# Kernel tuning notes

Measured on AMD Instinct MI355X. Metric: run time of the kernel, lower is better.

The kernel has to match this reference:

```python
import jax, jax.numpy as jnp
import numpy as np
from jax import lax

HIDDEN_DIM = 256


def _conv(x, w, b, stride):
    # x: [B,T,H,W,Cin], w: [1,kh,kw,Cin,Cout]
    y = lax.conv_general_dilated(
        x, w, window_strides=(1, stride, stride), padding='SAME',
        dimension_numbers=('NDHWC', 'DHWIO', 'NDHWC'))
    return y + b


def _encode(video, w1, b1, w2, b2, w3, b3):
    x = video / 255.0
    x = jax.nn.relu(_conv(x, w1, b1, 2))
    x = jax.nn.relu(_conv(x, w2, b2, 2))
    x = jax.nn.relu(_conv(x, w3, b3, 2))
    return x  # [B,T,H/8,W/8,HIDDEN_DIM]


def _sample_features(features, t_idx, y_idx, x_idx):
    # Bilinear sample features[b, t_idx, y_idx, x_idx] -> [B,N,C]
    B, T, H, W, C = features.shape
    t = jnp.clip(t_idx, 0, T - 1)
    y0 = jnp.clip(jnp.floor(y_idx).astype(jnp.int32), 0, H - 1)
    y1 = jnp.clip(y0 + 1, 0, H - 1)
    x0 = jnp.clip(jnp.floor(x_idx).astype(jnp.int32), 0, W - 1)
    x1 = jnp.clip(x0 + 1, 0, W - 1)
    wy1 = y_idx - y0.astype(features.dtype)
    wy0 = 1.0 - wy1
    wx1 = x_idx - x0.astype(features.dtype)
    wx0 = 1.0 - wx1
    bi = jnp.arange(B)[:, None]
    f00 = features[bi, t, y0, x0]
    f01 = features[bi, t, y0, x1]
    f10 = features[bi, t, y1, x0]
    f11 = features[bi, t, y1, x1]
    f0 = f00 * wx0[..., None] + f01 * wx1[..., None]
    f1 = f10 * wx0[..., None] + f11 * wx1[..., None]
    return f0 * wy0[..., None] + f1 * wy1[..., None]


def _forward(video, query_points, w1, b1, w2, b2, w3, b3):
    B, T, H, W, _ = video.shape
    N = query_points.shape[1]
    x = _encode(video, w1, b1, w2, b2, w3, b3)
    feat_H, feat_W = x.shape[2], x.shape[3]
    query_t = (query_points[:, :, 0] * (T - 1)).astype(jnp.int32)
    query_y = query_points[:, :, 1] * (feat_H - 1)
    query_x = query_points[:, :, 2] * (feat_W - 1)
    q = _sample_features(x, query_t, query_y, query_x)  # [B,N,C]
    # dense correlation volume [B,N,T,fH,fW]
    corr = jnp.einsum('bnc,bthwc->bnthw', q, x) / jnp.sqrt(jnp.float32(HIDDEN_DIM))
    probs = jax.nn.softmax(corr.reshape(B, N, T, feat_H * feat_W) * 10.0, axis=-1)
    yy, xx = jnp.meshgrid(jnp.arange(feat_H, dtype=x.dtype),
                          jnp.arange(feat_W, dtype=x.dtype), indexing='ij')
    coords_flat = jnp.stack([xx.flatten(), yy.flatten()], axis=-1)  # [fH*fW, 2]
    pred = jnp.einsum('bntk,kc->bntc', probs, coords_flat)
    pred = pred.at[..., 0].set(pred[..., 0] * (W / feat_W))
    pred = pred.at[..., 1].set(pred[..., 1] * (H / feat_H))
    occlusion = jax.nn.sigmoid(-jnp.max(corr, axis=(-2, -1)))  # [B,N,T]
    return pred, occlusion


def setup_inputs() -> dict:
    key = jax.random.key(0)
    ks = jax.random.split(key, 10)
    B, T, H, W, N = 2, 24, 256, 256, 512
    video = jax.random.uniform(ks[0], (B, T, H, W, 3), jnp.float32) * 255.0
    query_points = jax.random.uniform(ks[1], (B, N, 3), jnp.float32)
    s = 0.05
    w1 = jax.random.normal(ks[2], (1, 7, 7, 3, 64), jnp.float32) * s
    b1 = jnp.zeros((64,), jnp.float32)
    w2 = jax.random.normal(ks[3], (1, 3, 3, 64, 128), jnp.float32) * s
    b2 = jnp.zeros((128,), jnp.float32)
    w3 = jax.random.normal(ks[4], (1, 3, 3, 128, HIDDEN_DIM), jnp.float32) * s
    b3 = jnp.zeros((HIDDEN_DIM,), jnp.float32)
    return {'video': video, 'query_points': query_points,
            'w1': w1, 'b1': b1, 'w2': w2, 'b2': b2, 'w3': w3, 'b3': b3}


def reference(video, query_points, w1, b1, w2, b2, w3, b3):
    return _forward(video, query_points, w1, b1, w2, b2, w3, b3)
```

## Files before the change

### kernel.cpp

```cpp
#include <hip/hip_runtime.h>
#include <hip/hip_bf16.h>
#include <cstdint>
#include <cstddef>


typedef __attribute__((ext_vector_type(8))) short bf16x8;
typedef __attribute__((ext_vector_type(4))) float f32x4;

typedef const __attribute__((address_space(1))) void gv_t;
typedef __attribute__((address_space(3))) void sv_t;

__device__ __forceinline__ unsigned short bfr(float f) {
    return (unsigned short)(__bfloat16_as_ushort(__float2bfloat16(f)));
}

__global__ __launch_bounds__(256) void k_prep(const float* __restrict__ video,
                                              const float* __restrict__ w1,
                                              const float* __restrict__ w2,
                                              const float* __restrict__ w3,
                                              __hip_bfloat16* __restrict__ pv,
                                              unsigned short* __restrict__ c2p,
                                              __hip_bfloat16* __restrict__ wp1,
                                              __hip_bfloat16* __restrict__ wp2,
                                              __hip_bfloat16* __restrict__ wp3)
{
    const int bid = blockIdx.x;
    if (bid < 12288) {
        const int xcd = bid & 7;
        const int sub = bid >> 3;
        const int bt  = xcd * 6 + (sub >> 8);
        const int iy  = sub & 255;
        const int ix = threadIdx.x;
        const float* src = video + ((size_t)(bt * 256 + iy) * 256 + ix) * 3;
        unsigned* dst = (unsigned*)(pv + ((size_t)(bt * 261) + iy + 2) * 1056);
        const float v0 = src[0], v1 = src[1], v2 = src[2];
        const unsigned lo = (unsigned)bfr(v0) | ((unsigned)bfr(v1) << 16);
        const unsigned hi = (unsigned)bfr(v2);
        dst[(2 + ix) * 2 + 0] = lo;
        dst[(2 + ix) * 2 + 1] = hi;
        if (ix < 2)   { dst[ix * 2] = 0u; dst[ix * 2 + 1] = 0u; }
        if (ix >= 250){ dst[(ix + 8) * 2] = 0u; dst[(ix + 8) * 2 + 1] = 0u; }
    } else if (bid < 12288 + 4086) {
        const int i = (bid - 12288) * 256 + threadIdx.x;
        unsigned short* pvs = (unsigned short*)pv;
        if (i < 253440) {
            const int bt = i / 5280, rr = (i % 5280) / 1056, col = i % 1056;
            const int row = (rr < 2) ? rr : rr + 256;
            pvs[(size_t)(bt * 261 + row) * 1056 + col] = 0;
        } else {
            const int j = i - 253440, bt = j / 16512, k = j % 16512;
            size_t addr;
            if (k < 8320) { const int px = k >> 7, c = k & 127;
                addr = ((size_t)(bt * 65 + 64) * 65 + px) * 128 + c; }
            else { const int k2 = k - 8320, row = k2 >> 7, c = k2 & 127;
                addr = ((size_t)(bt * 65 + row) * 65 + 64) * 128 + c; }
            c2p[addr] = 0;
        }
    } else {
        const int e = (bid - 12288 - 4086) * 256 + threadIdx.x;
        if (e < 14336) {
            const int j = e & 7, lane = (e >> 3) & 63, nt = (e >> 9) & 3, kh = e >> 11;
            const int k = ((lane >> 4) << 3) + j;
            const int kw = k >> 2, ci = k & 3;
            const int n = nt * 16 + (lane & 15);
            float v = (ci < 3 && kw < 7) ? w1[(size_t)((kh * 7 + kw) * 3 + ci) * 64 + n] : 0.f;
            wp1[e] = __float2bfloat16(v);
        } else if (e < 88064) {
            const int e2 = e - 14336;
            const int j = e2 & 7, lane = (e2 >> 3) & 63, nt = (e2 >> 9) & 7, ks = (e2 >> 12) & 1, tap = e2 >> 13;
            const int ci = ks * 32 + ((lane >> 4) << 3) + j;
            const int n  = nt * 16 + (lane & 15);
            wp2[e2] = __float2bfloat16(w2[(size_t)(tap * 64 + ci) * 128 + n]);
        } else {
            const int e3 = e - 88064;
            const int j = e3 & 7, lane = (e3 >> 3) & 63, nt = (e3 >> 9) & 15, ks = (e3 >> 13) & 3, tap = e3 >> 15;
            const int ci = ks * 32 + ((lane >> 4) << 3) + j;
            const int n  = nt * 16 + (lane & 15);
            wp3[e3] = __float2bfloat16(w3[(size_t)(tap * 128 + ci) * 256 + n]);
        }
    }
}

__global__ __launch_bounds__(256, 2) void k_conv12(const __hip_bfloat16* __restrict__ pv,
                                                   const __hip_bfloat16* __restrict__ w1p,
                                                   const float* __restrict__ b1,
                                                   const __hip_bfloat16* __restrict__ w2p,
                                                   const float* __restrict__ b2,
                                                   __hip_bfloat16* __restrict__ c2p)
{
    __shared__ __align__(16) char lc1[3 * 16512];

    const int xcd = blockIdx.x & 7;
    const int sub = blockIdx.x >> 3;
    const int bt  = xcd * 6 + sub / 64;
    const int oy2 = sub % 64;
    const int tid = threadIdx.x;
    const int w   = tid >> 6;
    const int l   = tid & 63;
    const int li  = l & 15, lh = l >> 4;

    const short* pvS = (const short*)pv;
    const short* w1S = (const short*)w1p;

    const int r0 = oy2 * 2;
    f32x4 acc1[3][2][4];
#pragma unroll
    for (int row = 0; row < 3; ++row)
#pragma unroll
        for (int m = 0; m < 2; ++m)
#pragma unroll
            for (int n = 0; n < 4; ++n) acc1[row][m][n] = (f32x4){0.f, 0.f, 0.f, 0.f};

    const int ox0 = w * 32;
#pragma unroll
    for (int kh = 0; kh < 7; ++kh) {
        bf16x8 bw[4];
#pragma unroll
        for (int nt = 0; nt < 4; ++nt)
            bw[nt] = *reinterpret_cast<const bf16x8*>(w1S + ((size_t)(kh * 4 + nt) * 64 + l) * 8);
#pragma unroll
        for (int row = 0; row < 3; ++row) {
            const int r   = r0 + row;
            const int rcl = (r < 128) ? r : 127;
            const short* rbase = pvS + (size_t)(bt * 261 + rcl * 2 + kh) * 1056;
#pragma unroll
            for (int mt = 0; mt < 2; ++mt) {
                bf16x8 a = *reinterpret_cast<const bf16x8*>(
                    rbase + 8 * (ox0 + mt * 16 + li + lh));
#pragma unroll
                for (int nt = 0; nt < 4; ++nt)
                    acc1[row][mt][nt] = __builtin_amdgcn_mfma_f32_16x16x32_bf16(
                        a, bw[nt], acc1[row][mt][nt], 0, 0, 0);
            }
        }
    }

#pragma unroll
    for (int row = 0; row < 3; ++row) {
        const int r = r0 + row;
        char* rowbuf = lc1 + row * 16512;
        if (r < 128) {
#pragma unroll
            for (int mt = 0; mt < 2; ++mt) {
#pragma unroll
                for (int nt = 0; nt < 4; ++nt) {
                    const int n = nt * 16 + li;
                    const float bias = b1[n];
                    const int jg = nt * 2 + (li >> 3);
#pragma unroll
                    for (int r4 = 0; r4 < 4; ++r4) {
                        const int px = ox0 + mt * 16 + lh * 4 + r4;
                        const float v = fmaxf(acc1[row][mt][nt][r4] * (1.f / 255.f) + bias, 0.f);
                        *reinterpret_cast<unsigned short*>(
                            rowbuf + px * 128 + ((jg ^ ((px >> 1) & 7)) * 16 + (li & 7) * 2)) = bfr(v);
                    }
                }
            }
            if (tid < 8)
                *reinterpret_cast<uint4*>(rowbuf + 128 * 128 + tid * 16) = (uint4){0u, 0u, 0u, 0u};
        } else {
#pragma unroll
            for (int it = 0; it < 5; ++it) {
                const int g = it * 256 + tid;
                if (g < 1032)
                    *reinterpret_cast<uint4*>(rowbuf + (size_t)g * 16) = (uint4){0u, 0u, 0u, 0u};
            }
        }
    }
    __syncthreads();

    const int ntb = w * 2;
    f32x4 acc[4][2];
#pragma unroll
    for (int i = 0; i < 4; ++i) {
        acc[i][0] = (f32x4){0.f, 0.f, 0.f, 0.f};
        acc[i][1] = (f32x4){0.f, 0.f, 0.f, 0.f};
    }

    const char* wB = (const char*)w2p;
#pragma unroll
    for (int s = 0; s < 18; ++s) {
        const int tap = s >> 1, ks = s & 1;
        const int kh = tap / 3, kw = tap % 3;

        bf16x8 bf[2];
#pragma unroll
        for (int j = 0; j < 2; ++j)
            bf[j] = *reinterpret_cast<const bf16x8*>(wB + ((size_t)s * 8 + ntb + j) * 1024 + l * 16);

        const char* Ar = lc1 + kh * 16512;
        bf16x8 af[4];
#pragma unroll
        for (int i = 0; i < 4; ++i) {
            const int ix  = (i * 16 + li) * 2 + kw;
            const int off = ((ks * 4 + lh) ^ ((ix >> 1) & 7)) * 16;
            af[i] = *reinterpret_cast<const bf16x8*>(Ar + (size_t)ix * 128 + off);
        }

#pragma unroll
        for (int i = 0; i < 4; ++i)
#pragma unroll
            for (int j = 0; j < 2; ++j)
                acc[i][j] = __builtin_amdgcn_mfma_f32_16x16x32_bf16(af[i], bf[j], acc[i][j], 0, 0, 0);
    }

    __hip_bfloat16* ob = c2p + (size_t)(bt * 65 + oy2) * 65 * 128;
#pragma unroll
    for (int i = 0; i < 4; ++i) {
        const int ox = i * 16 + lh * 4;
#pragma unroll
        for (int j = 0; j < 2; ++j) {
            const int n = (ntb + j) * 16 + li;
            const float bv = b2[n];
#pragma unroll
            for (int r4 = 0; r4 < 4; ++r4) {
                const float v = fmaxf(acc[i][j][r4] + bv, 0.f);
                ob[(size_t)(ox + r4) * 128 + n] = __float2bfloat16(v);
            }
        }
    }
}

template<int CIN, int COUT, int OW, int IW, int ORS, int NTHR, int WMT, int WNT, int MINW>
__global__ __launch_bounds__(NTHR, MINW) void k_convr(const __hip_bfloat16* __restrict__ in,
                                                      const __hip_bfloat16* __restrict__ wp,
                                                      const float* __restrict__ bias,
                                                      __hip_bfloat16* __restrict__ out)
{
    constexpr int KSN  = CIN / 32;
    constexpr int NSL  = 9 * KSN;
    constexpr int NTT  = COUT / 16;
    constexpr int GPX  = CIN / 8;
    constexpr int ROWG = IW * GPX;
    constexpr int RST  = ROWG * 16;
    constexpr int TOT  = 3 * ROWG;
    constexpr int SIT  = (TOT + NTHR - 1) / NTHR;

    __shared__ char lbuf[3 * RST];

    const int bid = blockIdx.x;
    const int xcd = bid & 7;
    const int sub = bid >> 3;
    const int bt  = xcd * 6 + sub / OW;
    const int oy  = sub % OW;

    const int tid = threadIdx.x;
    const int w   = tid >> 6;
    const int l   = tid & 63;
    const int li  = l & 15, lh = l >> 4;
    const int ntb = w * WNT;

    const short* inS = (const short*)in;
    const size_t rb = (size_t)(bt * IW + oy * 2) * IW * CIN;
#pragma unroll
    for (int it = 0; it < SIT; ++it) {
        const int g = it * NTHR + tid;
        if (g < TOT) {
            const int r  = g / ROWG;
            const int rm = g - r * ROWG;
            const int px = rm / GPX;
            const int j  = rm - px * GPX;
            const int q  = j ^ ((px >> 1) & 7);
            __builtin_amdgcn_global_load_lds(
                (gv_t*)(inS + rb + (size_t)r * IW * CIN + px * CIN + q * 8),
                (sv_t*)(lbuf + (size_t)g * 16), 16, 0, 0);
        }
    }
    __syncthreads();

    f32x4 acc[WMT][WNT];
#pragma unroll
    for (int i = 0; i < WMT; ++i)
#pragma unroll
        for (int j = 0; j < WNT; ++j) acc[i][j] = (f32x4){0.f, 0.f, 0.f, 0.f};

    const char* wB = (const char*)wp;

#pragma unroll
    for (int s = 0; s < NSL; ++s) {
        const int tap = s / KSN, ks = s % KSN;
        const int kh = tap / 3, kw = tap % 3;

        bf16x8 bf[WNT];
#pragma unroll
        for (int j = 0; j < WNT; ++j)
            bf[j] = *reinterpret_cast<const bf16x8*>(wB + ((size_t)s * NTT + ntb + j) * 1024 + l * 16);

        const char* Ar = lbuf + kh * RST;
        bf16x8 af[WMT];
#pragma unroll
        for (int i = 0; i < WMT; ++i) {
            const int ix  = (i * 16 + li) * 2 + kw;
            const int off = ((ks * 4 + lh) ^ ((ix >> 1) & 7)) * 16;
            af[i] = *reinterpret_cast<const bf16x8*>(Ar + (size_t)ix * (CIN * 2) + off);
        }

#pragma unroll
        for (int i = 0; i < WMT; ++i)
#pragma unroll
            for (int j = 0; j < WNT; ++j)
                acc[i][j] = __builtin_amdgcn_mfma_f32_16x16x32_bf16(af[i], bf[j], acc[i][j], 0, 0, 0);
    }

    __hip_bfloat16* ob = out + (size_t)(bt * ORS + oy) * ORS * COUT;
#pragma unroll
    for (int i = 0; i < WMT; ++i) {
        const int ox = i * 16 + lh * 4;
#pragma unroll
        for (int j = 0; j < WNT; ++j) {
            const int n = (ntb + j) * 16 + li;
            const float bv = bias[n];
#pragma unroll
            for (int r = 0; r < 4; ++r) {
                const float v = fmaxf(acc[i][j][r] + bv, 0.f);
                ob[(size_t)(ox + r) * COUT + n] = __float2bfloat16(v);
            }
        }
    }
}

__global__ __launch_bounds__(256) void k_sample(const float* __restrict__ qp,
                                                const __hip_bfloat16* __restrict__ feat,
                                                __hip_bfloat16* __restrict__ q)
{
    const int bn = blockIdx.x;
    const int b  = bn >> 9;
    const float t3 = qp[bn * 3 + 0];
    const float yv = qp[bn * 3 + 1] * 31.f;
    const float xv = qp[bn * 3 + 2] * 31.f;
    int t = (int)(t3 * 23.f);
    t = min(max(t, 0), 23);
    int y0 = (int)floorf(yv); y0 = min(max(y0, 0), 31);
    const int y1 = min(y0 + 1, 31);
    int x0 = (int)floorf(xv); x0 = min(max(x0, 0), 31);
    const int x1 = min(x0 + 1, 31);
    const float wy1 = yv - (float)y0, wy0 = 1.f - wy1;
    const float wx1 = xv - (float)x0, wx0 = 1.f - wx1;

    const int c = threadIdx.x;
    const __hip_bfloat16* fb = feat + ((size_t)(b * 24 + t) * 1024) * 256;
    const float f00 = __bfloat162float(fb[(size_t)(y0 * 32 + x0) * 256 + c]);
    const float f01 = __bfloat162float(fb[(size_t)(y0 * 32 + x1) * 256 + c]);
    const float f10 = __bfloat162float(fb[(size_t)(y1 * 32 + x0) * 256 + c]);
    const float f11 = __bfloat162float(fb[(size_t)(y1 * 32 + x1) * 256 + c]);
    const float v = (f00 * wx0 + f01 * wx1) * wy0 + (f10 * wx0 + f11 * wx1) * wy1;
    q[(size_t)bn * 256 + c] = __float2bfloat16(v);
}

__global__ __launch_bounds__(256, 2) void k_corrm(const __hip_bfloat16* __restrict__ qb,
                                                  const __hip_bfloat16* __restrict__ featb,
                                                  float* __restrict__ pbuf)
{
    __shared__ short lbuf[2][8192];

    const int bid = blockIdx.x;
    const int xcd = bid & 7;
    const int sub = bid >> 3;
    const int grp = sub >> 5;
    const int prt = sub & 31;
    const int img = xcd * 6 + grp;
    const int bq  = img / 24, t = img % 24;
    const int nc  = prt & 3, ps = prt >> 2;

    const int tid = threadIdx.x;
    const int w   = tid >> 6;
    const int l   = tid & 63;
    const int li  = l & 15, lh = l >> 4;

    const short* qS = (const short*)qb;
    const short* fS = (const short*)featb + (size_t)img * 1024 * 256;
    const char*  tile0 = (const char*)(fS + (size_t)(ps * 128) * 256);

    const int q0 = nc * 128 + w * 32;
    bf16x8 aq[2][8];
#pragma unroll
    for (int mt = 0; mt < 2; ++mt)
#pragma unroll
        for (int ks = 0; ks < 8; ++ks)
            aq[mt][ks] = *reinterpret_cast<const bf16x8*>(
                qS + ((size_t)(bq * 512 + q0 + mt * 16 + li)) * 256 + ks * 32 + lh * 8);

    float m[2][4], s[2][4], sx[2][4], sy[2][4], dmx[2][4];
#pragma unroll
    for (int mt = 0; mt < 2; ++mt)
#pragma unroll
        for (int r = 0; r < 4; ++r) {
            m[mt][r] = -1e30f; s[mt][r] = 0.f; sx[mt][r] = 0.f; sy[mt][r] = 0.f; dmx[mt][r] = -1e30f;
        }

    bf16x8 stg[4];
#pragma unroll
    for (int i = 0; i < 4; ++i) {
        const int g = i * 256 + tid;
        const int pos = g >> 5, kb = (g & 31) * 16;
        stg[i] = *reinterpret_cast<const bf16x8*>(tile0 + (size_t)pos * 512 + kb);
    }
#pragma unroll
    for (int i = 0; i < 4; ++i) {
        const int g = i * 256 + tid;
        const int pos = g >> 5, kb = (g & 31) * 16;
        *reinterpret_cast<bf16x8*>((char*)&lbuf[0][0] + pos * 512 + (kb ^ ((pos & 7) << 4))) = stg[i];
    }
    __syncthreads();

#pragma unroll
    for (int st = 0; st < 4; ++st) {
        const int cur = st & 1;

        if (st < 3) {
            const char* tn = tile0 + (size_t)((st + 1) * 32) * 512;
#pragma unroll
            for (int i = 0; i < 4; ++i) {
                const int g = i * 256 + tid;
                const int pos = g >> 5, kb = (g & 31) * 16;
                stg[i] = *reinterpret_cast<const bf16x8*>(tn + (size_t)pos * 512 + kb);
            }
        }

        f32x4 acc[2][2];
#pragma unroll
        for (int mt = 0; mt < 2; ++mt)
#pragma unroll
            for (int pt = 0; pt < 2; ++pt) acc[mt][pt] = (f32x4){0.f, 0.f, 0.f, 0.f};

#pragma unroll
        for (int pt = 0; pt < 2; ++pt) {
            const int p = pt * 16 + li;
#pragma unroll
            for (int ks = 0; ks < 8; ++ks) {
                const int k = ks * 32 + lh * 8;
                bf16x8 bv = *reinterpret_cast<const bf16x8*>(&lbuf[cur][p * 256 + (k ^ ((p & 7) << 3))]);
                acc[0][pt] = __builtin_amdgcn_mfma_f32_16x16x32_bf16(aq[0][ks], bv, acc[0][pt], 0, 0, 0);
                acc[1][pt] = __builtin_amdgcn_mfma_f32_16x16x32_bf16(aq[1][ks], bv, acc[1][pt], 0, 0, 0);
            }
        }

        const float py = (float)(ps * 4 + st);
#pragma unroll
        for (int mt = 0; mt < 2; ++mt)
#pragma unroll
            for (int r = 0; r < 4; ++r) {
                const float v0 = acc[mt][0][r], v1 = acc[mt][1][r];
                float mx = fmaxf(v0, v1);
                mx = fmaxf(mx, __shfl_xor(mx, 1));
                mx = fmaxf(mx, __shfl_xor(mx, 2));
                mx = fmaxf(mx, __shfl_xor(mx, 4));
                mx = fmaxf(mx, __shfl_xor(mx, 8));
                dmx[mt][r] = fmaxf(dmx[mt][r], mx);
                const float mn = fmaxf(m[mt][r], mx * 0.625f);
                const float sc = __expf(m[mt][r] - mn);
                const float e0 = __expf(v0 * 0.625f - mn);
                const float e1 = __expf(v1 * 0.625f - mn);
                const float es = e0 + e1;
                s[mt][r]  = s[mt][r]  * sc + es;
                sx[mt][r] = sx[mt][r] * sc + es * (float)li + 16.f * e1;
                sy[mt][r] = sy[mt][r] * sc + es * py;
                m[mt][r] = mn;
            }

        if (st < 3) {
#pragma unroll
            for (int i = 0; i < 4; ++i) {
                const int g = i * 256 + tid;
                const int pos = g >> 5, kb = (g & 31) * 16;
                *reinterpret_cast<bf16x8*>((char*)&lbuf[cur ^ 1][0] + pos * 512 + (kb ^ ((pos & 7) << 4))) = stg[i];
            }
            __syncthreads();
        }
    }

#pragma unroll
    for (int mt = 0; mt < 2; ++mt)
#pragma unroll
        for (int r = 0; r < 4; ++r) {
#pragma unroll
            for (int off = 1; off < 16; off <<= 1) {
                s[mt][r]  += __shfl_xor(s[mt][r],  off);
                sx[mt][r] += __shfl_xor(sx[mt][r], off);
                sy[mt][r] += __shfl_xor(sy[mt][r], off);
            }
        }

    if (li == 0) {
#pragma unroll
        for (int mt = 0; mt < 2; ++mt)
#pragma unroll
            for (int r = 0; r < 4; ++r) {
                const int n = q0 + mt * 16 + lh * 4 + r;
                const int bnt = (bq * 512 + n) * 24 + t;
                const int pi = ps * 24576 + bnt;
                pbuf[pi]                = m[mt][r];
                pbuf[196608 + pi]       = s[mt][r];
                pbuf[393216 + pi]       = sx[mt][r];
                pbuf[589824 + pi]       = sy[mt][r];
                pbuf[786432 + pi]       = dmx[mt][r];
            }
    }
}

__global__ __launch_bounds__(256) void k_merge(const float* __restrict__ pbuf,
                                               float* __restrict__ outp)
{
    const int i = blockIdx.x * 256 + threadIdx.x;
    float M = -1e30f, D = -1e30f;
#pragma unroll
    for (int ps = 0; ps < 8; ++ps) {
        M = fmaxf(M, pbuf[ps * 24576 + i]);
        D = fmaxf(D, pbuf[786432 + ps * 24576 + i]);
    }
    float s = 0.f, sx = 0.f, sy = 0.f;
#pragma unroll
    for (int ps = 0; ps < 8; ++ps) {
        const int pi = ps * 24576 + i;
        const float wgt = __expf(pbuf[pi] - M);
        s  += pbuf[196608 + pi] * wgt;
        sx += pbuf[393216 + pi] * wgt;
        sy += pbuf[589824 + pi] * wgt;
    }
    const float inv = 8.f / s;
    outp[i * 2 + 0] = sx * inv;
    outp[i * 2 + 1] = sy * inv;
    outp[49152 + i] = 1.f / (1.f + __expf(D * 0.0625f));
}

extern "C" void kernel_launch(void* const* d_in, const int* in_sizes, int n_in,
                              void* d_out, int out_size, void* d_ws, size_t ws_size,
                              hipStream_t stream)
{
    const float* video = (const float*)d_in[0];
    const float* qp    = (const float*)d_in[1];
    const float* w1    = (const float*)d_in[2];
    const float* b1    = (const float*)d_in[3];
    const float* w2    = (const float*)d_in[4];
    const float* b2    = (const float*)d_in[5];
    const float* w3    = (const float*)d_in[6];
    const float* b3    = (const float*)d_in[7];
    float* out = (float*)d_out;

    char* wsb = (char*)d_ws;
    __hip_bfloat16* c2p   = (__hip_bfloat16*)(wsb);
    __hip_bfloat16* pv    = (__hip_bfloat16*)(wsb + 51916800ull);
    __hip_bfloat16* featb = (__hip_bfloat16*)(wsb + 51916800ull);
    __hip_bfloat16* qbuf  = (__hip_bfloat16*)(wsb + 78375936ull);
    __hip_bfloat16* w1p   = (__hip_bfloat16*)(wsb + 78900224ull);
    __hip_bfloat16* w2p   = (__hip_bfloat16*)(wsb + 78928896ull);
    __hip_bfloat16* w3p   = (__hip_bfloat16*)(wsb + 79076352ull);
    float*          pbuf  = (float*)(wsb + 79666176ull);

    k_prep   <<<dim3(17870), dim3(256), 0, stream>>>(
                  video, w1, w2, w3, pv, (unsigned short*)c2p, w1p, w2p, w3p);
    k_conv12 <<<dim3(3072),  dim3(256), 0, stream>>>(pv, w1p, b1, w2p, b2, c2p);
    k_convr<128, 256, 32, 65, 32, 512, 2, 2, 6><<<dim3(1536), dim3(512), 0, stream>>>(c2p, w3p, b3, featb);
    k_sample <<<dim3(1024),  dim3(256), 0, stream>>>(qp, featb, qbuf);
    k_corrm  <<<dim3(1536),  dim3(256), 0, stream>>>(qbuf, featb, pbuf);
    k_merge  <<<dim3(96),    dim3(256), 0, stream>>>(pbuf, out);
}
```

Before: 169.5 us.

## Reuse two LDS row buffers in conv12 to raise occupancy to three blocks

Shrinks the conv1 output staging buffer from three rows to two by processing conv2 kernel rows in phases: rows 0 and 1 are written, row 0 is consumed, then its buffer is overwritten with row 2 while row 1 is consumed. The launch bound is raised from 2 to 3 blocks per CU, which the smaller LDS footprint allows. The aim is more concurrent waves to hide latency, at the cost of two extra barriers and tighter register limits that could cause spills given the large accumulator arrays.

```diff
diff --git a/kernel.cpp b/kernel.cpp
--- a/kernel.cpp
+++ b/kernel.cpp
@@ -81,14 +81,14 @@
     }
 }
 
-__global__ __launch_bounds__(256, 2) void k_conv12(const __hip_bfloat16* __restrict__ pv,
+__global__ __launch_bounds__(256, 3) void k_conv12(const __hip_bfloat16* __restrict__ pv,
                                                    const __hip_bfloat16* __restrict__ w1p,
                                                    const float* __restrict__ b1,
                                                    const __hip_bfloat16* __restrict__ w2p,
                                                    const float* __restrict__ b2,
                                                    __hip_bfloat16* __restrict__ c2p)
 {
-    __shared__ __align__(16) char lc1[3 * 16512];
+    __shared__ __align__(16) char lc1[2][16512];
 
     const int xcd = blockIdx.x & 7;
     const int sub = blockIdx.x >> 3;
@@ -135,39 +135,34 @@
         }
     }
 
-#pragma unroll
-    for (int row = 0; row < 3; ++row) {
-        const int r = r0 + row;
-        char* rowbuf = lc1 + row * 16512;
-        if (r < 128) {
-#pragma unroll
-            for (int mt = 0; mt < 2; ++mt) {
-#pragma unroll
-                for (int nt = 0; nt < 4; ++nt) {
-                    const int n = nt * 16 + li;
-                    const float bias = b1[n];
-                    const int jg = nt * 2 + (li >> 3);
-#pragma unroll
-                    for (int r4 = 0; r4 < 4; ++r4) {
-                        const int px = ox0 + mt * 16 + lh * 4 + r4;
-                        const float v = fmaxf(acc1[row][mt][nt][r4] * (1.f / 255.f) + bias, 0.f);
-                        *reinterpret_cast<unsigned short*>(
-                            rowbuf + px * 128 + ((jg ^ ((px >> 1) & 7)) * 16 + (li & 7) * 2)) = bfr(v);
-                    }
+    auto wrow = [&](const f32x4 (&ar)[2][4], char* rowbuf) {
+#pragma unroll
+        for (int mt = 0; mt < 2; ++mt) {
+#pragma unroll
+            for (int nt = 0; nt < 4; ++nt) {
+                const int n = nt * 16 + li;
+                const float bias = b1[n];
+                const int jg = nt * 2 + (li >> 3);
+#pragma unroll
+                for (int r4 = 0; r4 < 4; ++r4) {
+                    const int px = ox0 + mt * 16 + lh * 4 + r4;
+                    const float v = fmaxf(ar[mt][nt][r4] * (1.f / 255.f) + bias, 0.f);
+                    *reinterpret_cast<unsigned short*>(
+                        rowbuf + px * 128 + ((jg ^ ((px >> 1) & 7)) * 16 + (li & 7) * 2)) = bfr(v);
                 }
             }
-            if (tid < 8)
-                *reinterpret_cast<uint4*>(rowbuf + 128 * 128 + tid * 16) = (uint4){0u, 0u, 0u, 0u};
-        } else {
-#pragma unroll
-            for (int it = 0; it < 5; ++it) {
-                const int g = it * 256 + tid;
-                if (g < 1032)
-                    *reinterpret_cast<uint4*>(rowbuf + (size_t)g * 16) = (uint4){0u, 0u, 0u, 0u};
-            }
-        }
-    }
-    __syncthreads();
+        }
+        if (tid < 8)
+            *reinterpret_cast<uint4*>(rowbuf + 128 * 128 + tid * 16) = (uint4){0u, 0u, 0u, 0u};
+    };
+    auto zrow = [&](char* rowbuf) {
+#pragma unroll
+        for (int it = 0; it < 5; ++it) {
+            const int g = it * 256 + tid;
+            if (g < 1032)
+                *reinterpret_cast<uint4*>(rowbuf + (size_t)g * 16) = (uint4){0u, 0u, 0u, 0u};
+        }
+    };
 
     const int ntb = w * 2;
     f32x4 acc[4][2];
@@ -176,33 +171,45 @@
         acc[i][0] = (f32x4){0.f, 0.f, 0.f, 0.f};
         acc[i][1] = (f32x4){0.f, 0.f, 0.f, 0.f};
     }
-
     const char* wB = (const char*)w2p;
-#pragma unroll
-    for (int s = 0; s < 18; ++s) {
-        const int tap = s >> 1, ks = s & 1;
-        const int kh = tap / 3, kw = tap % 3;
-
-        bf16x8 bf[2];
-#pragma unroll
-        for (int j = 0; j < 2; ++j)
-            bf[j] = *reinterpret_cast<const bf16x8*>(wB + ((size_t)s * 8 + ntb + j) * 1024 + l * 16);
-
-        const char* Ar = lc1 + kh * 16512;
-        bf16x8 af[4];
-#pragma unroll
-        for (int i = 0; i < 4; ++i) {
-            const int ix  = (i * 16 + li) * 2 + kw;
-            const int off = ((ks * 4 + lh) ^ ((ix >> 1) & 7)) * 16;
-            af[i] = *reinterpret_cast<const bf16x8*>(Ar + (size_t)ix * 128 + off);
-        }
-
-#pragma unroll
-        for (int i = 0; i < 4; ++i)
+
+    auto p2 = [&](int kh, const char* Ar) {
+#pragma unroll
+        for (int sub6 = 0; sub6 < 6; ++sub6) {
+            const int kw = sub6 >> 1, ks = sub6 & 1;
+            const int s  = (kh * 3 + kw) * 2 + ks;
+
+            bf16x8 bf[2];
 #pragma unroll
             for (int j = 0; j < 2; ++j)
-                acc[i][j] = __builtin_amdgcn_mfma_f32_16x16x32_bf16(af[i], bf[j], acc[i][j], 0, 0, 0);
-    }
+                bf[j] = *reinterpret_cast<const bf16x8*>(wB + ((size_t)s * 8 + ntb + j) * 1024 + l * 16);
+
+            bf16x8 af[4];
+#pragma unroll
+            for (int i = 0; i < 4; ++i) {
+                const int ix  = (i * 16 + li) * 2 + kw;
+                const int off = ((ks * 4 + lh) ^ ((ix >> 1) & 7)) * 16;
+                af[i] = *reinterpret_cast<const bf16x8*>(Ar + (size_t)ix * 128 + off);
+            }
+
+#pragma unroll
+            for (int i = 0; i < 4; ++i)
+#pragma unroll
+                for (int j = 0; j < 2; ++j)
+                    acc[i][j] = __builtin_amdgcn_mfma_f32_16x16x32_bf16(af[i], bf[j], acc[i][j], 0, 0, 0);
+        }
+    };
+
+    wrow(acc1[0], lc1[0]);
+    wrow(acc1[1], lc1[1]);
+    __syncthreads();
+    p2(0, lc1[0]);
+    __syncthreads();
+    if (r0 + 2 < 128) wrow(acc1[2], lc1[0]);
+    else              zrow(lc1[0]);
+    p2(1, lc1[1]);
+    __syncthreads();
+    p2(2, lc1[0]);
 
     __hip_bfloat16* ob = c2p + (size_t)(bt * 65 + oy2) * 65 * 128;
 #pragma unroll
```

New measurement: 188.5 us. 1.11x slower.
